# Optimization experiments

Hardware: AMD Instinct MI355X
Metric: run time of the kernel (lower is better)

Reference implementation:

```python
import jax, jax.numpy as jnp
import numpy as np


def setup_inputs() -> dict:
    key = jax.random.key(0)
    k1, k2, k3 = jax.random.split(key, 3)
    N, S = 65536, 128  # rays, samples per ray
    # t: sorted sample distances along each ray (near=2.0, far=6.0 typical NeRF bounds)
    t = jnp.sort(jax.random.uniform(k1, (N, S, 1), jnp.float32, 2.0, 6.0), axis=-2)
    # sigma: non-negative densities (post-ReLU/softplus output of NerfDensity)
    sigma = jax.random.uniform(k2, (N, S, 1), jnp.float32, 0.0, 2.0)
    # color: RGB in [0,1] (post-sigmoid output of NerfColor)
    color = jax.random.uniform(k3, (N, S, 3), jnp.float32, 0.0, 1.0)
    return {"t": t, "sigma": sigma, "color": color}


def integrate_ray(t, sigma, color, infinite=False):
    # t, sigma: [N, S, 1]; color: [N, S, 3]
    dt = t[..., 1:, :] - t[..., :-1, :]                      # [N, S-1, 1]
    last = 1e10 * jnp.ones_like(dt[..., 0:1, :]) if infinite else jnp.zeros_like(dt[..., 0:1, :])
    dt = jnp.concatenate((dt, last), axis=-2)                # [N, S, 1]
    sdt = sigma * dt                                         # [N, S, 1]
    Ti = jnp.exp(-jnp.cumsum(sdt, axis=-2))[..., 0:-1, :]    # transmittance, shifted
    Ti = jnp.concatenate((jnp.ones_like(Ti[..., 0:1, :]), Ti), axis=-2)
    alpha = 1.0 - jnp.exp(-sdt)
    wi = Ti * alpha                                          # [N, S, 1]
    return ((wi * color).sum(axis=-2), (wi * t).sum(axis=-2), wi, t)


def reference(t, sigma, color):
    # forward(): t is sorted along the sample dim before integration.
    t = jnp.sort(t, axis=-2)
    return integrate_ray(t, sigma, color, infinite=False)
```

## Files before the change

kernel.cpp:

```cpp
#include <hip/hip_runtime.h>
#include <math.h>


#define NRAYS 65536
#define S 128
#define RAYS_PER_BLOCK 8

typedef float __attribute__((ext_vector_type(4))) fvec4;

__global__ __launch_bounds__(256) void nerf_integrate_kernel(
    const float* __restrict__ t,
    const float* __restrict__ sigma,
    const float* __restrict__ color,
    float* __restrict__ out_color,
    float* __restrict__ out_depth,
    float* __restrict__ out_wi)
{
    const int lane    = threadIdx.x & 63;
    const int seglane = lane & 31;
    const int wave    = threadIdx.x >> 6;
    const int ray = blockIdx.x * RAYS_PER_BLOCK + wave * 2 + (lane >> 5);

    const long sbase = (long)ray * S + 4 * seglane;

    const fvec4 tv = __builtin_nontemporal_load((const fvec4*)(t + sbase));
    const fvec4 sv = __builtin_nontemporal_load((const fvec4*)(sigma + sbase));
    const fvec4* cp = (const fvec4*)(color + (long)ray * (S * 3) + 12 * seglane);
    const fvec4 c0 = __builtin_nontemporal_load(cp + 0);
    const fvec4 c1 = __builtin_nontemporal_load(cp + 1);
    const fvec4 c2 = __builtin_nontemporal_load(cp + 2);

    const float t_next = __shfl_down(tv.x, 1, 32);
    const float dt0 = tv.y - tv.x;
    const float dt1 = tv.z - tv.y;
    const float dt2 = tv.w - tv.z;
    const float dt3 = (seglane == 31) ? 0.0f : (t_next - tv.w);

    const float p0  = sv.x * dt0;
    const float p1  = p0 + sv.y * dt1;
    const float p2  = p1 + sv.z * dt2;
    const float tot = p2 + sv.w * dt3;

    float scan = tot;
    #pragma unroll
    for (int off = 1; off < 32; off <<= 1) {
        const float v = __shfl_up(scan, off, 32);
        if (seglane >= off) scan += v;
    }
    const float excl = scan - tot;

    const float E0 = __expf(-excl);
    const float e0 = __expf(-(excl + p0));
    const float e1 = __expf(-(excl + p1));
    const float e2 = __expf(-(excl + p2));
    const float e3 = __expf(-scan);
    const float wi0 = E0 - e0;
    const float wi1 = e0 - e1;
    const float wi2 = e1 - e2;
    const float wi3 = e2 - e3;

    fvec4 wiv; wiv.x = wi0; wiv.y = wi1; wiv.z = wi2; wiv.w = wi3;
    __builtin_nontemporal_store(wiv, (fvec4*)(out_wi + sbase));

    float r = wi0 * c0.x + wi1 * c0.w + wi2 * c1.z + wi3 * c2.y;
    float g = wi0 * c0.y + wi1 * c1.x + wi2 * c1.w + wi3 * c2.z;
    float b = wi0 * c0.z + wi1 * c1.y + wi2 * c2.x + wi3 * c2.w;
    float d = wi0 * tv.x + wi1 * tv.y + wi2 * tv.z + wi3 * tv.w;

    #pragma unroll
    for (int off = 16; off >= 1; off >>= 1) {
        r += __shfl_xor(r, off, 32);
        g += __shfl_xor(g, off, 32);
        b += __shfl_xor(b, off, 32);
        d += __shfl_xor(d, off, 32);
    }

    if (seglane == 0) {
        out_color[(long)ray * 3 + 0] = r;
        out_color[(long)ray * 3 + 1] = g;
        out_color[(long)ray * 3 + 2] = b;
        out_depth[ray] = d;
    }
}

#define COPY_BLOCKS 2048
#define COPY_VEC4   (NRAYS * S / 4)

__global__ __launch_bounds__(256) void nerf_tcopy_kernel(
    const float* __restrict__ t,
    float* __restrict__ out_t)
{
    const fvec4* src = (const fvec4*)t;
    fvec4* dst = (fvec4*)out_t;
    const int stride = COPY_BLOCKS * 256;
    int idx = blockIdx.x * 256 + threadIdx.x;
    #pragma unroll
    for (int i = 0; i < COPY_VEC4 / (COPY_BLOCKS * 256); ++i) {
        const fvec4 v = __builtin_nontemporal_load(src + idx);
        __builtin_nontemporal_store(v, dst + idx);
        idx += stride;
    }
}

extern "C" void kernel_launch(void* const* d_in, const int* in_sizes, int n_in,
                              void* d_out, int out_size, void* d_ws, size_t ws_size,
                              hipStream_t stream) {
    const float* t     = (const float*)d_in[0];
    const float* sigma = (const float*)d_in[1];
    const float* color = (const float*)d_in[2];

    float* out = (float*)d_out;
    float* out_color = out;
    float* out_depth = out_color + (long)NRAYS * 3;
    float* out_wi    = out_depth + NRAYS;
    float* out_t     = out_wi + (long)NRAYS * S;

    nerf_tcopy_kernel<<<COPY_BLOCKS, 256, 0, stream>>>(t, out_t);

    const int blocks = NRAYS / RAYS_PER_BLOCK;
    nerf_integrate_kernel<<<blocks, 256, 0, stream>>>(
        t, sigma, color, out_color, out_depth, out_wi);
}
```

Before: 212.0 us.

## Fuse t copy into integrate kernel and stage color through LDS

Removes the separate t copy kernel and writes out_t from the t vector already loaded in the integrate kernel, so t is read from global memory once instead of twice. Color is loaded with fully coalesced block-wide vector loads into shared memory, then redistributed per ray. This adds a __syncthreads and 12KB LDS per block, which may reduce occupancy slightly.

```diff
diff --git a/kernel.cpp b/kernel.cpp
--- a/kernel.cpp
+++ b/kernel.cpp
@@ -8,27 +8,44 @@
 
 typedef float __attribute__((ext_vector_type(4))) fvec4;
 
-__global__ __launch_bounds__(256) void nerf_integrate_kernel(
+__global__ __launch_bounds__(256) void nerf_fused_kernel(
     const float* __restrict__ t,
     const float* __restrict__ sigma,
     const float* __restrict__ color,
     float* __restrict__ out_color,
     float* __restrict__ out_depth,
-    float* __restrict__ out_wi)
+    float* __restrict__ out_wi,
+    float* __restrict__ out_t)
 {
-    const int lane    = threadIdx.x & 63;
+    __shared__ fvec4 lds_c[RAYS_PER_BLOCK * S * 3 / 4];
+
+    const int tid     = threadIdx.x;
+    const int lane    = tid & 63;
     const int seglane = lane & 31;
-    const int wave    = threadIdx.x >> 6;
-    const int ray = blockIdx.x * RAYS_PER_BLOCK + wave * 2 + (lane >> 5);
+    const int seg     = tid >> 5;
+    const int ray     = blockIdx.x * RAYS_PER_BLOCK + seg;
 
     const long sbase = (long)ray * S + 4 * seglane;
 
+    const fvec4* gc = (const fvec4*)(color + (long)blockIdx.x * (RAYS_PER_BLOCK * S * 3));
+    const fvec4 g0 = __builtin_nontemporal_load(gc + tid);
+    const fvec4 g1 = __builtin_nontemporal_load(gc + tid + 256);
+    const fvec4 g2 = __builtin_nontemporal_load(gc + tid + 512);
+
     const fvec4 tv = __builtin_nontemporal_load((const fvec4*)(t + sbase));
     const fvec4 sv = __builtin_nontemporal_load((const fvec4*)(sigma + sbase));
-    const fvec4* cp = (const fvec4*)(color + (long)ray * (S * 3) + 12 * seglane);
-    const fvec4 c0 = __builtin_nontemporal_load(cp + 0);
-    const fvec4 c1 = __builtin_nontemporal_load(cp + 1);
-    const fvec4 c2 = __builtin_nontemporal_load(cp + 2);
+
+    __builtin_nontemporal_store(tv, (fvec4*)(out_t + sbase));
+
+    lds_c[tid]       = g0;
+    lds_c[tid + 256] = g1;
+    lds_c[tid + 512] = g2;
+    __syncthreads();
+
+    const int cidx = seg * (S * 3 / 4) + 3 * seglane;
+    const fvec4 c0 = lds_c[cidx + 0];
+    const fvec4 c1 = lds_c[cidx + 1];
+    const fvec4 c2 = lds_c[cidx + 2];
 
     const float t_next = __shfl_down(tv.x, 1, 32);
     const float dt0 = tv.y - tv.x;
@@ -83,25 +100,6 @@
     }
 }
 
-#define COPY_BLOCKS 2048
-#define COPY_VEC4   (NRAYS * S / 4)
-
-__global__ __launch_bounds__(256) void nerf_tcopy_kernel(
-    const float* __restrict__ t,
-    float* __restrict__ out_t)
-{
-    const fvec4* src = (const fvec4*)t;
-    fvec4* dst = (fvec4*)out_t;
-    const int stride = COPY_BLOCKS * 256;
-    int idx = blockIdx.x * 256 + threadIdx.x;
-    #pragma unroll
-    for (int i = 0; i < COPY_VEC4 / (COPY_BLOCKS * 256); ++i) {
-        const fvec4 v = __builtin_nontemporal_load(src + idx);
-        __builtin_nontemporal_store(v, dst + idx);
-        idx += stride;
-    }
-}
-
 extern "C" void kernel_launch(void* const* d_in, const int* in_sizes, int n_in,
                               void* d_out, int out_size, void* d_ws, size_t ws_size,
                               hipStream_t stream) {
@@ -115,9 +113,7 @@
     float* out_wi    = out_depth + NRAYS;
     float* out_t     = out_wi + (long)NRAYS * S;
 
-    nerf_tcopy_kernel<<<COPY_BLOCKS, 256, 0, stream>>>(t, out_t);
-
     const int blocks = NRAYS / RAYS_PER_BLOCK;
-    nerf_integrate_kernel<<<blocks, 256, 0, stream>>>(
-        t, sigma, color, out_color, out_depth, out_wi);
+    nerf_fused_kernel<<<blocks, 256, 0, stream>>>(
+        t, sigma, color, out_color, out_depth, out_wi, out_t);
 }
```

Result: faster. 197.8 us (-6.7%).
